# Optimization experiments

Hardware: AMD Instinct MI355X
Metric: run time of the kernel (lower is better)

## Reference

```python
import jax, jax.numpy as jnp
import numpy as np

ALPHABET = 4      # DNA symbols 0..3
PAD_SYMBOL = 4    # outside alphabet
PAD_LENGTH = 2048 # = 2*N, worst-case compacted length
B, N = 8192, 1024


def setup_inputs() -> dict:
    key = jax.random.key(0)
    k1, k2, k3, k4 = jax.random.split(key, 4)
    x = jax.random.randint(k1, (B, N, 1), 0, ALPHABET, dtype=jnp.int32)
    # IDS category per position: 0=insertion, 1=deletion, 2=substitution, 3=clean
    mask = jax.random.randint(k2, (B, N), 0, 4, dtype=jnp.int32)
    # random symbols used where an insertion occurs (both repeated slots)
    ins_rand = jax.random.randint(k3, (B, 2 * N), 0, ALPHABET, dtype=jnp.int32)
    # substitution offset - 1; reference adds 1 so offset is in [1, ALPHABET)
    sub_off = jax.random.randint(k4, (B, 2 * N), 0, ALPHABET - 1, dtype=jnp.int32)
    return {"x": x, "mask": mask, "ins_rand": ins_rand, "sub_off": sub_off}


def reference(x, mask, ins_rand, sub_off):
    # x: [B, N, 1] int32; mask: [B, N]; ins_rand, sub_off: [B, 2N]
    b, n, _ = x.shape
    mask_rep = jnp.repeat(mask, 2, axis=1)        # [B, 2N]
    x_rep = jnp.repeat(x[..., 0], 2, axis=1)      # [B, 2N]
    # insertion: both repeated slots replaced by uniform random symbols
    x_i = jnp.where(mask_rep == 0, ins_rand, x_rep)
    # substitution: add offset in [1, ALPHABET) mod ALPHABET
    x_is = jnp.where(mask_rep == 2, (x_i + sub_off + 1) % ALPHABET, x_i)
    even = (jnp.arange(2 * n) % 2 == 0)[None, :]  # even slots of the doubled axis
    keep = (((mask_rep == 3) & even)              # clean: keep one copy
            | (mask_rep == 0)                     # insertion: keep both copies
            | ((mask_rep == 2) & even))           # substitution: keep one copy
    # vectorized stream compaction via prefix-sum + OOB-dropping scatter
    pos = jnp.cumsum(keep.astype(jnp.int32), axis=1) - 1   # target index if kept
    idx = jnp.where(keep, pos, PAD_LENGTH)                 # PAD_LENGTH -> dropped
    out = jnp.full((b, PAD_LENGTH), PAD_SYMBOL, dtype=x.dtype)
    out = out.at[jnp.arange(b)[:, None], idx].set(x_is, mode='drop')
    return out[..., None]                                  # [B, PAD_LENGTH, 1]
```

## Files before the change

### kernel.cpp

```cpp
#include <hip/hip_runtime.h>

#define NPOS 1024
#define OUTLEN 2048
#define PAD_SYM 4
#define WAVES_PER_BLOCK 4
#define ROWB 2176

typedef int iv4 __attribute__((ext_vector_type(4)));

__global__ __launch_bounds__(256) void ids_gallager_kernel(
    const int* __restrict__ x, const int* __restrict__ mask,
    const int* __restrict__ ins_rand, const int* __restrict__ sub_off,
    int* __restrict__ out, int B)
{
    __shared__ alignas(16) unsigned char lds[WAVES_PER_BLOCK][ROWB];

    const int wave = (int)(blockIdx.x * WAVES_PER_BLOCK + (threadIdx.x >> 6));
    const int w    = (int)(threadIdx.x >> 6);
    const int lane = (int)(threadIdx.x & 63);
    if (wave >= B) return;

    const int4* mv  = (const int4*)(mask     + (size_t)wave * NPOS);
    const int4* xv  = (const int4*)(x        + (size_t)wave * NPOS);
    const int4* ivv = (const int4*)(ins_rand + (size_t)wave * OUTLEN);
    const int4* svv = (const int4*)(sub_off  + (size_t)wave * OUTLEN);
    int* outr = out + (size_t)wave * OUTLEN;

    unsigned char* row   = lds[w];
    int*           row32 = (int*)row;
    const int dump = OUTLEN + lane;

    int carry = 0;
#pragma unroll
    for (int c = 0; c < 4; ++c) {
        const int4 mt = mv[c * 64 + lane];
        const int4 xt = xv[c * 64 + lane];
        const int4 i0 = ivv[c * 128 + 2 * lane];
        const int4 i1 = ivv[c * 128 + 2 * lane + 1];
        const int4 s0 = svv[c * 128 + 2 * lane];
        const int4 s1 = svv[c * 128 + 2 * lane + 1];

        const int mm[4] = { mt.x, mt.y, mt.z, mt.w };
        const int xx[4] = { xt.x, xt.y, xt.z, xt.w };
        const int iA[4] = { i0.x, i0.z, i1.x, i1.z };
        const int iB[4] = { i0.y, i0.w, i1.y, i1.w };
        const int sO[4] = { s0.x, s0.z, s1.x, s1.z };

        int cnt = 0;
#pragma unroll
        for (int k = 0; k < 4; ++k)
            cnt += (mm[k] == 0) ? 2 : ((mm[k] == 1) ? 0 : 1);

        int incl = cnt;
#pragma unroll
        for (int d = 1; d < 64; d <<= 1) {
            int t = __shfl_up(incl, d, 64);
            if (lane >= d) incl += t;
        }
        int p = carry + incl - cnt;
        carry += __shfl(incl, 63, 64);

#pragma unroll
        for (int k = 0; k < 4; ++k) {
            const int m_  = mm[k];
            const int cc  = (m_ == 0) ? 2 : ((m_ == 1) ? 0 : 1);
            const int sub = (xx[k] + sO[k] + 1) & 3;
            const int e0  = (m_ == 0) ? iA[k] : ((m_ == 2) ? sub : xx[k]);
            row[(cc != 0) ? p       : dump] = (unsigned char)e0;
            row[(cc == 2) ? (p + 1) : dump] = (unsigned char)iB[k];
            p += cc;
        }
    }
    const int total = carry;

    const int a4 = (total + 3) & ~3;
    if (lane < a4 - total) row[total + lane] = (unsigned char)PAD_SYM;
    for (int j4 = (a4 >> 2) + lane; j4 < (OUTLEN >> 2); j4 += 64)
        row32[j4] = 0x04040404;

    __syncthreads();

#pragma unroll
    for (int k = 0; k < 8; ++k) {
        const unsigned int d = *(const unsigned int*)(row + k * 256 + lane * 4);
        iv4 v;
        v.x = (int)(d & 0xffu);
        v.y = (int)((d >> 8)  & 0xffu);
        v.z = (int)((d >> 16) & 0xffu);
        v.w = (int)(d >> 24);
        __builtin_nontemporal_store(v, (iv4*)(outr + k * 256 + lane * 4));
    }
}

extern "C" void kernel_launch(void* const* d_in, const int* in_sizes, int n_in,
                              void* d_out, int out_size, void* d_ws, size_t ws_size,
                              hipStream_t stream) {
    const int* x        = (const int*)d_in[0];
    const int* mask     = (const int*)d_in[1];
    const int* ins_rand = (const int*)d_in[2];
    const int* sub_off  = (const int*)d_in[3];
    int* out            = (int*)d_out;

    const int B = in_sizes[1] / NPOS;
    const int blocks = (B + WAVES_PER_BLOCK - 1) / WAVES_PER_BLOCK;
    ids_gallager_kernel<<<blocks, 256, 0, stream>>>(x, mask, ins_rand, sub_off, out, B);
}
```

Measured before the change: 42.64 us.

## Process each row with a full block using cross-wave prefix scan

```diff
diff --git a/kernel.cpp b/kernel.cpp
--- a/kernel.cpp
+++ b/kernel.cpp
@@ -3,8 +3,7 @@
 #define NPOS 1024
 #define OUTLEN 2048
 #define PAD_SYM 4
-#define WAVES_PER_BLOCK 4
-#define ROWB 2176
+#define ROWB (OUTLEN + 256)
 
 typedef int iv4 __attribute__((ext_vector_type(4)));
 
@@ -13,82 +12,87 @@
     const int* __restrict__ ins_rand, const int* __restrict__ sub_off,
     int* __restrict__ out, int B)
 {
-    __shared__ alignas(16) unsigned char lds[WAVES_PER_BLOCK][ROWB];
+    __shared__ alignas(16) unsigned char row[ROWB];
+    __shared__ int wtot[4];
 
-    const int wave = (int)(blockIdx.x * WAVES_PER_BLOCK + (threadIdx.x >> 6));
-    const int w    = (int)(threadIdx.x >> 6);
-    const int lane = (int)(threadIdx.x & 63);
-    if (wave >= B) return;
+    const int rowi = (int)blockIdx.x;
+    if (rowi >= B) return;
+    const int tid  = (int)threadIdx.x;
+    const int lane = tid & 63;
+    const int w    = tid >> 6;
 
-    const int4* mv  = (const int4*)(mask     + (size_t)wave * NPOS);
-    const int4* xv  = (const int4*)(x        + (size_t)wave * NPOS);
-    const int4* ivv = (const int4*)(ins_rand + (size_t)wave * OUTLEN);
-    const int4* svv = (const int4*)(sub_off  + (size_t)wave * OUTLEN);
-    int* outr = out + (size_t)wave * OUTLEN;
+    const int4* mv  = (const int4*)(mask     + (size_t)rowi * NPOS);
+    const int4* xv  = (const int4*)(x        + (size_t)rowi * NPOS);
+    const int4* ivv = (const int4*)(ins_rand + (size_t)rowi * OUTLEN);
+    const int4* svv = (const int4*)(sub_off  + (size_t)rowi * OUTLEN);
+    int* outr = out + (size_t)rowi * OUTLEN;
 
-    unsigned char* row   = lds[w];
-    int*           row32 = (int*)row;
-    const int dump = OUTLEN + lane;
+    int* row32 = (int*)row;
+    const int dump = OUTLEN + tid;
 
-    int carry = 0;
+    const int4 mt = mv[tid];
+    const int4 xt = xv[tid];
+    const int4 i0 = ivv[2 * tid];
+    const int4 i1 = ivv[2 * tid + 1];
+    const int4 s0 = svv[2 * tid];
+    const int4 s1 = svv[2 * tid + 1];
+
+    const int mm[4] = { mt.x, mt.y, mt.z, mt.w };
+    const int xx[4] = { xt.x, xt.y, xt.z, xt.w };
+    const int iA[4] = { i0.x, i0.z, i1.x, i1.z };
+    const int iB[4] = { i0.y, i0.w, i1.y, i1.w };
+    const int sO[4] = { s0.x, s0.z, s1.x, s1.z };
+
+    int cnt = 0;
 #pragma unroll
-    for (int c = 0; c < 4; ++c) {
-        const int4 mt = mv[c * 64 + lane];
-        const int4 xt = xv[c * 64 + lane];
-        const int4 i0 = ivv[c * 128 + 2 * lane];
-        const int4 i1 = ivv[c * 128 + 2 * lane + 1];
-        const int4 s0 = svv[c * 128 + 2 * lane];
-        const int4 s1 = svv[c * 128 + 2 * lane + 1];
+    for (int k = 0; k < 4; ++k)
+        cnt += (mm[k] == 0) ? 2 : ((mm[k] == 1) ? 0 : 1);
 
-        const int mm[4] = { mt.x, mt.y, mt.z, mt.w };
-        const int xx[4] = { xt.x, xt.y, xt.z, xt.w };
-        const int iA[4] = { i0.x, i0.z, i1.x, i1.z };
-        const int iB[4] = { i0.y, i0.w, i1.y, i1.w };
-        const int sO[4] = { s0.x, s0.z, s1.x, s1.z };
+    int incl = cnt;
+#pragma unroll
+    for (int d = 1; d < 64; d <<= 1) {
+        int t = __shfl_up(incl, d, 64);
+        if (lane >= d) incl += t;
+    }
+    if (lane == 63) wtot[w] = incl;
+    __syncthreads();
 
-        int cnt = 0;
+    int prefix = 0, total = 0;
 #pragma unroll
-        for (int k = 0; k < 4; ++k)
-            cnt += (mm[k] == 0) ? 2 : ((mm[k] == 1) ? 0 : 1);
-
-        int incl = cnt;
-#pragma unroll
-        for (int d = 1; d < 64; d <<= 1) {
-            int t = __shfl_up(incl, d, 64);
-            if (lane >= d) incl += t;
-        }
-        int p = carry + incl - cnt;
-        carry += __shfl(incl, 63, 64);
+    for (int i = 0; i < 4; ++i) {
+        const int t = wtot[i];
+        prefix += (i < w) ? t : 0;
+        total  += t;
+    }
+    int p = prefix + incl - cnt;
 
 #pragma unroll
-        for (int k = 0; k < 4; ++k) {
-            const int m_  = mm[k];
-            const int cc  = (m_ == 0) ? 2 : ((m_ == 1) ? 0 : 1);
-            const int sub = (xx[k] + sO[k] + 1) & 3;
-            const int e0  = (m_ == 0) ? iA[k] : ((m_ == 2) ? sub : xx[k]);
-            row[(cc != 0) ? p       : dump] = (unsigned char)e0;
-            row[(cc == 2) ? (p + 1) : dump] = (unsigned char)iB[k];
-            p += cc;
-        }
+    for (int k = 0; k < 4; ++k) {
+        const int m_  = mm[k];
+        const int cc  = (m_ == 0) ? 2 : ((m_ == 1) ? 0 : 1);
+        const int sub = (xx[k] + sO[k] + 1) & 3;
+        const int e0  = (m_ == 0) ? iA[k] : ((m_ == 2) ? sub : xx[k]);
+        row[(cc != 0) ? p       : dump] = (unsigned char)e0;
+        row[(cc == 2) ? (p + 1) : dump] = (unsigned char)iB[k];
+        p += cc;
     }
-    const int total = carry;
 
     const int a4 = (total + 3) & ~3;
-    if (lane < a4 - total) row[total + lane] = (unsigned char)PAD_SYM;
-    for (int j4 = (a4 >> 2) + lane; j4 < (OUTLEN >> 2); j4 += 64)
+    if (tid < a4 - total) row[total + tid] = (unsigned char)PAD_SYM;
+    for (int j4 = (a4 >> 2) + tid; j4 < (OUTLEN >> 2); j4 += 256)
         row32[j4] = 0x04040404;
 
     __syncthreads();
 
 #pragma unroll
-    for (int k = 0; k < 8; ++k) {
-        const unsigned int d = *(const unsigned int*)(row + k * 256 + lane * 4);
+    for (int k = 0; k < 2; ++k) {
+        const unsigned int d = *(const unsigned int*)(row + k * 1024 + tid * 4);
         iv4 v;
         v.x = (int)(d & 0xffu);
         v.y = (int)((d >> 8)  & 0xffu);
         v.z = (int)((d >> 16) & 0xffu);
         v.w = (int)(d >> 24);
-        __builtin_nontemporal_store(v, (iv4*)(outr + k * 256 + lane * 4));
+        __builtin_nontemporal_store(v, (iv4*)(outr + k * 1024 + tid * 4));
     }
 }
 
@@ -102,6 +106,5 @@
     int* out            = (int*)d_out;
 
     const int B = in_sizes[1] / NPOS;
-    const int blocks = (B + WAVES_PER_BLOCK - 1) / WAVES_PER_BLOCK;
-    ids_gallager_kernel<<<blocks, 256, 0, stream>>>(x, mask, ins_rand, sub_off, out, B);
+    ids_gallager_kernel<<<B, 256, 0, stream>>>(x, mask, ins_rand, sub_off, out, B);
 }
```

Result: no change. 42.40 us (-0.6%).
